# Kernel tuning notes

Hardware: AMD Instinct MI355X
Metric: run time of the kernel (lower is better)

## Reference

```python
import jax, jax.numpy as jnp
import numpy as np

LEAKY_SLOPE = 0.2  # tf.nn.leaky_relu default alpha
NEG_INF = -1e9


def setup_inputs() -> dict:
    key = jax.random.key(0)
    k1, k2, k3, k4 = jax.random.split(key, 4)
    B, N, F, D, H = 1, 4096, 128, 64, 4
    features = jax.random.normal(k1, (B, N, F), dtype=jnp.float32)
    adj = jax.random.randint(k2, (N, N), 0, 2, dtype=jnp.int32)  # 0/1 adjacency
    W = jax.random.normal(k3, (H, F, D), dtype=jnp.float32) * 0.1
    attn_k = jax.random.normal(k4, (H, 2 * D, 1), dtype=jnp.float32) * 0.1
    return {"adj": adj, "features": features, "W": W, "attn_k": attn_k}


def reference(adj, features, W, attn_k):
    H, _, D = W.shape
    adj_f = adj.astype(jnp.float32)[None]       # [1, N, N], broadcast over batch
    mask = adj_f != 0.0
    outs = []
    for i in range(H):  # fixed small head loop (heads are structurally distinct weights)
        h = features @ W[i]                      # [B, N, D]
        a_self = h @ attn_k[i, :D]               # [B, N, 1]
        a_neigh = h @ attn_k[i, D:]              # [B, N, 1]
        scores = a_self + jnp.swapaxes(a_neigh, 1, 2)  # [B, N, N] additive scores
        scores = jax.nn.leaky_relu(scores, LEAKY_SLOPE)
        scores = jnp.where(mask, scores, NEG_INF)
        attn = jax.nn.softmax(scores, axis=-1)   # [B, N, N]
        outs.append((attn * adj_f) @ h)          # [B, N, D]
    out = jnp.concatenate(outs, axis=-1) if H > 1 else outs[0]
    return jax.nn.relu(out)
```

## Files before the change

kernel.cpp:

```cpp
#include <hip/hip_runtime.h>
#include <math.h>

#define NN 4096
#define FF 128
#define DD 64
#define HH 4
#define NC 256

typedef _Float16 f16x8 __attribute__((ext_vector_type(8)));
typedef _Float16 f16x4 __attribute__((ext_vector_type(4)));
typedef _Float16 f16x2 __attribute__((ext_vector_type(2)));
typedef float    f32x4 __attribute__((ext_vector_type(4)));

__global__ __launch_bounds__(256) void prep_kernel(
    const float* __restrict__ feats, const float* __restrict__ W,
    const float* __restrict__ ak, _Float16* __restrict__ Bpack,
    _Float16* __restrict__ Es, _Float16* __restrict__ Fs,
    _Float16* __restrict__ En, _Float16* __restrict__ Fn)
{
    __shared__ _Float16 Wth[64 * 136];
    __shared__ _Float16 fth[32 * 128];
    __shared__ float    hlds[32 * 65];
    const int t  = threadIdx.x;
    const int h  = blockIdx.y;
    const int n0 = blockIdx.x * 32;

    {
        const float* Wh = W + h * (FF * DD);
        #pragma unroll
        for (int j = 0; j < 8; ++j) {
            int idx = j * 256 + t;
            int f   = idx >> 4;
            int d4  = idx & 15;
            float4 v = ((const float4*)Wh)[idx];
            Wth[(d4 * 4 + 0) * 136 + f] = (_Float16)v.x;
            Wth[(d4 * 4 + 1) * 136 + f] = (_Float16)v.y;
            Wth[(d4 * 4 + 2) * 136 + f] = (_Float16)v.z;
            Wth[(d4 * 4 + 3) * 136 + f] = (_Float16)v.w;
        }
        #pragma unroll
        for (int j = 0; j < 4; ++j) {
            int idx = j * 256 + t;
            int r = idx >> 5, f4 = idx & 31;
            float4 v = ((const float4*)feats)[(size_t)(n0 + r) * 32 + f4];
            f16x4 hv = {(_Float16)v.x, (_Float16)v.y, (_Float16)v.z, (_Float16)v.w};
            *(f16x4*)&fth[r * 128 + f4 * 4] = hv;
        }
    }
    __syncthreads();

    const int d   = t & 63;
    const int wid = t >> 6;
    float acc[8];
    #pragma unroll
    for (int j = 0; j < 8; ++j) acc[j] = 0.f;

    union UW { f16x8 v; unsigned int u[4]; };
    for (int f8 = 0; f8 < 16; ++f8) {
        UW w8; w8.v = *(const f16x8*)&Wth[d * 136 + f8 * 8];
        #pragma unroll
        for (int j = 0; j < 8; ++j) {
            const int r = wid + 4 * j;
            UW fv; fv.v = *(const f16x8*)&fth[r * 128 + f8 * 8];
            #pragma unroll
            for (int p = 0; p < 4; ++p)
                acc[j] = __builtin_amdgcn_fdot2(
                    __builtin_bit_cast(f16x2, w8.u[p]),
                    __builtin_bit_cast(f16x2, fv.u[p]), acc[j], false);
        }
    }

    const float aks = ak[h * 128 + d];
    const float akn = ak[h * 128 + 64 + d];
    #pragma unroll
    for (int j = 0; j < 8; ++j) {
        const int r = wid + 4 * j;
        const float hv = acc[j];
        hlds[r * 65 + d] = hv;
        float v1 = hv * aks;
        float v2 = hv * akn;
        #pragma unroll
        for (int m = 32; m >= 1; m >>= 1) {
            v1 += __shfl_xor(v1, m, 64);
            v2 += __shfl_xor(v2, m, 64);
        }
        if (d == 0) {
            Es[h * NN + n0 + r] = (_Float16)__expf(v1);
            Fs[h * NN + n0 + r] = (_Float16)__expf(0.2f * v1);
            En[h * NN + n0 + r] = (_Float16)__expf(v2);
            Fn[h * NN + n0 + r] = (_Float16)__expf(0.2f * v2);
        }
    }
    __syncthreads();

    const int cb = t >> 6;
    const int l  = t & 63;
    const int lr = l & 15;
    const int kg = l >> 4;
    f16x8 v;
    #pragma unroll
    for (int j = 0; j < 8; ++j)
        v[j] = (_Float16)hlds[(kg * 8 + j) * 65 + cb * 16 + lr];
    *(f16x8*)(Bpack + ((size_t)(h * 128 + blockIdx.x)) * 2048 + (cb * 64 + l) * 8) = v;
}

__global__ __launch_bounds__(256, 4) void attn_kernel(
    const int* __restrict__ adj, const _Float16* __restrict__ Bpack,
    const _Float16* __restrict__ Es, const _Float16* __restrict__ Fs,
    const _Float16* __restrict__ En, const _Float16* __restrict__ Fn,
    float* __restrict__ pacc, float* __restrict__ pden, int ksplit)
{
    __shared__ _Float16 adjh[2][2][1024];

    const int t  = threadIdx.x;
    const int h  = t >> 6;
    const int l  = t & 63;
    const int lr = l & 15;
    const int kg = l >> 4;
    const int n0 = blockIdx.x * 32;
    const int s  = blockIdx.y;

    const int mstart = s * ksplit;
    const int nch    = ksplit >> 5;
    const int coff   = blockIdx.x & (nch - 1);
#define PCH(c) ((((c) + coff) & (nch - 1)))
#define CLC(c) ((c) < nch ? (c) : nch - 1)

    const _Float16 es0 = Es[h * NN + n0 + lr],      fs0 = Fs[h * NN + n0 + lr];
    const _Float16 es1 = Es[h * NN + n0 + 16 + lr], fs1 = Fs[h * NN + n0 + 16 + lr];
    const f16x2 es20 = {es0, es0}, fs20 = {fs0, fs0};
    const f16x2 es21 = {es1, es1}, fs21 = {fs1, fs1};

    const _Float16* __restrict__ EnB = En + (size_t)h * NN + mstart + kg * 8;
    const _Float16* __restrict__ FnB = Fn + (size_t)h * NN + mstart + kg * 8;
    const _Float16* __restrict__ bhead =
        Bpack + ((size_t)(h * 128) + (mstart >> 5)) * 2048 + l * 8;

    const int sr = t >> 3;
    const int mq = t & 7;
    const int swoff = sr * 32 + (((mq >> 1) ^ (sr & 3)) << 3) + (mq & 1) * 4;
    const int* __restrict__ adjRow = adj + (size_t)(n0 + sr) * NN + mstart;

    const int perm = kg ^ (lr & 3);
    const int ro0  = lr * 32 + perm * 8;
    const int ro1  = (lr + 16) * 32 + perm * 8;

    f32x4 acc[2][4] = {};
    f32x4 dacc[2]   = {};
    f16x8 ones;
    #pragma unroll
    for (int j = 0; j < 8; ++j) ones[j] = (_Float16)1.0f;

    union U8 { f16x8 v; unsigned int u[4]; };

#define LDADJ(DST, C) do {                                                    \
        DST = ((const int4*)(adjRow + PCH(CLC(C)) * 32))[mq];                 \
    } while (0)
#define STADJ(PB, SUB, SRC) do {                                              \
        f16x4 _hv = {(_Float16)(SRC.x != 0), (_Float16)(SRC.y != 0),          \
                     (_Float16)(SRC.z != 0), (_Float16)(SRC.w != 0)};         \
        *(f16x4*)&adjh[PB][SUB][swoff] = _hv;                                 \
    } while (0)
#define LOADB(DST, C) do {                                                    \
        const _Float16* _b = bhead + (size_t)PCH(CLC(C)) * 2048;              \
        _Pragma("unroll")                                                     \
        for (int _cb = 0; _cb < 4; ++_cb)                                     \
            DST[_cb] = *(const f16x8*)(_b + _cb * 512);                       \
    } while (0)
#define LOADT(EQ, FQ, C) do {                                                 \
        EQ = *(const uint4*)(EnB + PCH(CLC(C)) * 32);                         \
        FQ = *(const uint4*)(FnB + PCH(CLC(C)) * 32);                         \
    } while (0)

#define CHUNK(C, PB, SUB, BCUR, BNXT, EQC, FQC, EQN, FQN) do {                \
        LOADB(BNXT, (C) + 1);                                                 \
        LOADT(EQN, FQN, (C) + 1);                                             \
        U8 AM0, AM1;                                                          \
        AM0.v = *(const f16x8*)&adjh[PB][SUB][ro0];                           \
        AM1.v = *(const f16x8*)&adjh[PB][SUB][ro1];                           \
        U8 A0, A1;                                                            \
        _Pragma("unroll")                                                     \
        for (int p = 0; p < 4; ++p) {                                         \
            const unsigned int eu = p == 0 ? EQC.x : p == 1 ? EQC.y : p == 2 ? EQC.z : EQC.w; \
            const unsigned int fu = p == 0 ? FQC.x : p == 1 ? FQC.y : p == 2 ? FQC.z : FQC.w; \
            const f16x2 en2 = __builtin_bit_cast(f16x2, eu);                  \
            const f16x2 fn2 = __builtin_bit_cast(f16x2, fu);                  \
            const f16x2 a20 = __builtin_bit_cast(f16x2, AM0.u[p]);            \
            const f16x2 a21 = __builtin_bit_cast(f16x2, AM1.u[p]);            \
            const f16x2 v0 = __builtin_elementwise_max(es20 * en2, fs20 * fn2) * a20; \
            const f16x2 v1 = __builtin_elementwise_max(es21 * en2, fs21 * fn2) * a21; \
            A0.u[p] = __builtin_bit_cast(unsigned int, v0);                   \
            A1.u[p] = __builtin_bit_cast(unsigned int, v1);                   \
        }                                                                     \
        __builtin_amdgcn_s_setprio(1);                                        \
        _Pragma("unroll")                                                     \
        for (int _cb = 0; _cb < 4; ++_cb) {                                   \
            acc[0][_cb] = __builtin_amdgcn_mfma_f32_16x16x32_f16(A0.v, BCUR[_cb], acc[0][_cb], 0, 0, 0); \
            acc[1][_cb] = __builtin_amdgcn_mfma_f32_16x16x32_f16(A1.v, BCUR[_cb], acc[1][_cb], 0, 0, 0); \
        }                                                                     \
        dacc[0] = __builtin_amdgcn_mfma_f32_16x16x32_f16(A0.v, ones, dacc[0], 0, 0, 0); \
        dacc[1] = __builtin_amdgcn_mfma_f32_16x16x32_f16(A1.v, ones, dacc[1], 0, 0, 0); \
        __builtin_amdgcn_s_setprio(0);                                        \
    } while (0)

    f16x8 B_0[4], B_1[4];
    uint4 eq0, fq0, eq1, fq1;
    int4  aA, aB;

    LDADJ(aA, 0);
    LDADJ(aB, 1);
    STADJ(0, 0, aA);
    STADJ(0, 1, aB);
    LDADJ(aA, 2);
    LDADJ(aB, 3);
    LOADB(B_0, 0);
    LOADT(eq0, fq0, 0);
    __syncthreads();

    const int npair = nch >> 1;
    for (int k = 0; k < npair; ++k) {
        const int nb = (k + 1) & 1;
        const int pb = k & 1;
        STADJ(nb, 0, aA);
        STADJ(nb, 1, aB);
        LDADJ(aA, 2 * k + 4);
        LDADJ(aB, 2 * k + 5);

        CHUNK(2 * k,     pb, 0, B_0, B_1, eq0, fq0, eq1, fq1);
        CHUNK(2 * k + 1, pb, 1, B_1, B_0, eq1, fq1, eq0, fq0);

        __syncthreads();
    }
#undef CHUNK
#undef LOADT
#undef LOADB
#undef STADJ
#undef LDADJ
#undef CLC
#undef PCH

    #pragma unroll
    for (int rb = 0; rb < 2; ++rb) {
        #pragma unroll
        for (int r = 0; r < 4; ++r) {
            const int row = n0 + rb * 16 + kg * 4 + r;
            #pragma unroll
            for (int cb = 0; cb < 4; ++cb)
                pacc[((size_t)(s * NN + row)) * NC + h * 64 + cb * 16 + lr] = acc[rb][cb][r];
            if (lr == 0)
                pden[(s * NN + row) * 4 + h] = dacc[rb][r];
        }
    }
}

__global__ __launch_bounds__(256) void finalize_kernel(
    const float* __restrict__ pacc, const float* __restrict__ pden,
    float* __restrict__ out, int nsplit)
{
    const int t = threadIdx.x;
    const int n = blockIdx.x * 4 + (t >> 6);
    const int q = t & 63;
    const int h = q >> 4;

    f32x4 a = {0.f, 0.f, 0.f, 0.f};
    float d = 0.f;
    for (int s = 0; s < nsplit; ++s) {
        a += *(const f32x4*)&pacc[((size_t)(s * NN + n)) * NC + q * 4];
        d += pden[(s * NN + n) * 4 + h];
    }
    f32x4 o;
    const float inv = (d > 0.f) ? 1.0f / d : 0.f;
    #pragma unroll
    for (int i = 0; i < 4; ++i) {
        const float v = a[i] * inv;
        o[i] = v > 0.f ? v : 0.f;
    }
    *(f32x4*)&out[(size_t)n * NC + q * 4] = o;
}

extern "C" void kernel_launch(void* const* d_in, const int* in_sizes, int n_in,
                              void* d_out, int out_size, void* d_ws, size_t ws_size,
                              hipStream_t stream)
{
    const int*   adj   = (const int*)d_in[0];
    const float* feats = (const float*)d_in[1];
    const float* W     = (const float*)d_in[2];
    const float* ak    = (const float*)d_in[3];
    float*       out   = (float*)d_out;

    char* ws = (char*)d_ws;
    _Float16* Bpack = (_Float16*)ws;
    _Float16* Es    = (_Float16*)(ws + (2ull << 20));
    _Float16* Fs    = (_Float16*)(ws + (2ull << 20) + (1 << 15));
    _Float16* En    = (_Float16*)(ws + (2ull << 20) + (2 << 15));
    _Float16* Fn    = (_Float16*)(ws + (2ull << 20) + (3 << 15));
    float*    pden  = (float*)(ws + (2ull << 20) + (4 << 15));
    float*    pacc  = (float*)(ws + (3ull << 20));

    int nsplit = 8;
    while (nsplit > 1 && ws_size < (3ull << 20) + (size_t)nsplit * (4ull << 20))
        nsplit >>= 1;
    const int ksplit = NN / nsplit;

    prep_kernel<<<dim3(128, 4), 256, 0, stream>>>(feats, W, ak, Bpack, Es, Fs, En, Fn);
    attn_kernel<<<dim3(128, nsplit), 256, 0, stream>>>(adj, Bpack, Es, Fs, En, Fn,
                                                       pacc, pden, ksplit);
    finalize_kernel<<<1024, 256, 0, stream>>>(pacc, pden, out, nsplit);
}
```

Measured before the change: 57.14 us.

## Store split partials in fp16, deepen adjacency prefetch, and load B per chunk

Partial accumulators and denominators are now written as fp16 instead of fp32, which halves the split-K partial traffic and the workspace footprint. The exp factors are pre-scaled by 1/8 so the fp16 partials stay in range, and finalize reads 8 halves per thread over fewer blocks. The attention loop now keeps four adjacency register stages in flight instead of two, while B and exp-factor loads are issued inside each chunk with no register double-buffering. The changes risk fp16 precision loss in the partial sums and expose B-load latency to the MFMA chain, though they cut register pressure.

```diff
diff --git a/kernel.cpp b/kernel.cpp
--- a/kernel.cpp
+++ b/kernel.cpp
@@ -6,6 +6,7 @@
 #define DD 64
 #define HH 4
 #define NC 256
+#define TSCALE 0.125f
 
 typedef _Float16 f16x8 __attribute__((ext_vector_type(8)));
 typedef _Float16 f16x4 __attribute__((ext_vector_type(4)));
@@ -85,10 +86,10 @@
             v2 += __shfl_xor(v2, m, 64);
         }
         if (d == 0) {
-            Es[h * NN + n0 + r] = (_Float16)__expf(v1);
-            Fs[h * NN + n0 + r] = (_Float16)__expf(0.2f * v1);
-            En[h * NN + n0 + r] = (_Float16)__expf(v2);
-            Fn[h * NN + n0 + r] = (_Float16)__expf(0.2f * v2);
+            Es[h * NN + n0 + r] = (_Float16)(__expf(v1) * TSCALE);
+            Fs[h * NN + n0 + r] = (_Float16)(__expf(0.2f * v1) * TSCALE);
+            En[h * NN + n0 + r] = (_Float16)(__expf(v2) * TSCALE);
+            Fn[h * NN + n0 + r] = (_Float16)(__expf(0.2f * v2) * TSCALE);
         }
     }
     __syncthreads();
@@ -108,7 +109,7 @@
     const int* __restrict__ adj, const _Float16* __restrict__ Bpack,
     const _Float16* __restrict__ Es, const _Float16* __restrict__ Fs,
     const _Float16* __restrict__ En, const _Float16* __restrict__ Fn,
-    float* __restrict__ pacc, float* __restrict__ pden, int ksplit)
+    _Float16* __restrict__ pacc, _Float16* __restrict__ pden, int ksplit)
 {
     __shared__ _Float16 adjh[2][2][1024];
 
@@ -161,28 +162,23 @@
                      (_Float16)(SRC.z != 0), (_Float16)(SRC.w != 0)};         \
         *(f16x4*)&adjh[PB][SUB][swoff] = _hv;                                 \
     } while (0)
-#define LOADB(DST, C) do {                                                    \
+
+#define CHUNK(C, PB, SUB) do {                                                \
         const _Float16* _b = bhead + (size_t)PCH(CLC(C)) * 2048;              \
-        _Pragma("unroll")                                                     \
-        for (int _cb = 0; _cb < 4; ++_cb)                                     \
-            DST[_cb] = *(const f16x8*)(_b + _cb * 512);                       \
-    } while (0)
-#define LOADT(EQ, FQ, C) do {                                                 \
-        EQ = *(const uint4*)(EnB + PCH(CLC(C)) * 32);                         \
-        FQ = *(const uint4*)(FnB + PCH(CLC(C)) * 32);                         \
-    } while (0)
-
-#define CHUNK(C, PB, SUB, BCUR, BNXT, EQC, FQC, EQN, FQN) do {                \
-        LOADB(BNXT, (C) + 1);                                                 \
-        LOADT(EQN, FQN, (C) + 1);                                             \
+        f16x8 Bf0 = *(const f16x8*)(_b);                                      \
+        f16x8 Bf1 = *(const f16x8*)(_b + 512);                                \
+        f16x8 Bf2 = *(const f16x8*)(_b + 1024);                               \
+        f16x8 Bf3 = *(const f16x8*)(_b + 1536);                               \
+        const uint4 eq = *(const uint4*)(EnB + PCH(CLC(C)) * 32);             \
+        const uint4 fq = *(const uint4*)(FnB + PCH(CLC(C)) * 32);             \
         U8 AM0, AM1;                                                          \
         AM0.v = *(const f16x8*)&adjh[PB][SUB][ro0];                           \
         AM1.v = *(const f16x8*)&adjh[PB][SUB][ro1];                           \
         U8 A0, A1;                                                            \
         _Pragma("unroll")                                                     \
         for (int p = 0; p < 4; ++p) {                                         \
-            const unsigned int eu = p == 0 ? EQC.x : p == 1 ? EQC.y : p == 2 ? EQC.z : EQC.w; \
-            const unsigned int fu = p == 0 ? FQC.x : p == 1 ? FQC.y : p == 2 ? FQC.z : FQC.w; \
+            const unsigned int eu = p == 0 ? eq.x : p == 1 ? eq.y : p == 2 ? eq.z : eq.w; \
+            const unsigned int fu = p == 0 ? fq.x : p == 1 ? fq.y : p == 2 ? fq.z : fq.w; \
             const f16x2 en2 = __builtin_bit_cast(f16x2, eu);                  \
             const f16x2 fn2 = __builtin_bit_cast(f16x2, fu);                  \
             const f16x2 a20 = __builtin_bit_cast(f16x2, AM0.u[p]);            \
@@ -193,47 +189,52 @@
             A1.u[p] = __builtin_bit_cast(unsigned int, v1);                   \
         }                                                                     \
         __builtin_amdgcn_s_setprio(1);                                        \
-        _Pragma("unroll")                                                     \
-        for (int _cb = 0; _cb < 4; ++_cb) {                                   \
-            acc[0][_cb] = __builtin_amdgcn_mfma_f32_16x16x32_f16(A0.v, BCUR[_cb], acc[0][_cb], 0, 0, 0); \
-            acc[1][_cb] = __builtin_amdgcn_mfma_f32_16x16x32_f16(A1.v, BCUR[_cb], acc[1][_cb], 0, 0, 0); \
-        }                                                                     \
+        acc[0][0] = __builtin_amdgcn_mfma_f32_16x16x32_f16(A0.v, Bf0, acc[0][0], 0, 0, 0); \
+        acc[1][0] = __builtin_amdgcn_mfma_f32_16x16x32_f16(A1.v, Bf0, acc[1][0], 0, 0, 0); \
+        acc[0][1] = __builtin_amdgcn_mfma_f32_16x16x32_f16(A0.v, Bf1, acc[0][1], 0, 0, 0); \
+        acc[1][1] = __builtin_amdgcn_mfma_f32_16x16x32_f16(A1.v, Bf1, acc[1][1], 0, 0, 0); \
+        acc[0][2] = __builtin_amdgcn_mfma_f32_16x16x32_f16(A0.v, Bf2, acc[0][2], 0, 0, 0); \
+        acc[1][2] = __builtin_amdgcn_mfma_f32_16x16x32_f16(A1.v, Bf2, acc[1][2], 0, 0, 0); \
+        acc[0][3] = __builtin_amdgcn_mfma_f32_16x16x32_f16(A0.v, Bf3, acc[0][3], 0, 0, 0); \
+        acc[1][3] = __builtin_amdgcn_mfma_f32_16x16x32_f16(A1.v, Bf3, acc[1][3], 0, 0, 0); \
         dacc[0] = __builtin_amdgcn_mfma_f32_16x16x32_f16(A0.v, ones, dacc[0], 0, 0, 0); \
         dacc[1] = __builtin_amdgcn_mfma_f32_16x16x32_f16(A1.v, ones, dacc[1], 0, 0, 0); \
         __builtin_amdgcn_s_setprio(0);                                        \
     } while (0)
 
-    f16x8 B_0[4], B_1[4];
-    uint4 eq0, fq0, eq1, fq1;
-    int4  aA, aB;
-
-    LDADJ(aA, 0);
-    LDADJ(aB, 1);
-    STADJ(0, 0, aA);
-    STADJ(0, 1, aB);
-    LDADJ(aA, 2);
-    LDADJ(aB, 3);
-    LOADB(B_0, 0);
-    LOADT(eq0, fq0, 0);
+    int4 a0A, a0B, a1A, a1B, a2A, a2B, a3A, a3B;
+
+    LDADJ(a0A, 0); LDADJ(a0B, 1);
+    LDADJ(a1A, 2); LDADJ(a1B, 3);
+    LDADJ(a2A, 4); LDADJ(a2B, 5);
+    LDADJ(a3A, 6); LDADJ(a3B, 7);
+    STADJ(0, 0, a0A); STADJ(0, 1, a0B);
     __syncthreads();
 
     const int npair = nch >> 1;
-    for (int k = 0; k < npair; ++k) {
-        const int nb = (k + 1) & 1;
-        const int pb = k & 1;
-        STADJ(nb, 0, aA);
-        STADJ(nb, 1, aB);
-        LDADJ(aA, 2 * k + 4);
-        LDADJ(aB, 2 * k + 5);
-
-        CHUNK(2 * k,     pb, 0, B_0, B_1, eq0, fq0, eq1, fq1);
-        CHUNK(2 * k + 1, pb, 1, B_1, B_0, eq1, fq1, eq0, fq0);
-
+    for (int k = 0; k < npair; k += 4) {
+        STADJ(1, 0, a1A); STADJ(1, 1, a1B);
+        LDADJ(a0A, 2 * k + 8); LDADJ(a0B, 2 * k + 9);
+        CHUNK(2 * k,     0, 0);
+        CHUNK(2 * k + 1, 0, 1);
         __syncthreads();
+        STADJ(0, 0, a2A); STADJ(0, 1, a2B);
+        LDADJ(a1A, 2 * k + 10); LDADJ(a1B, 2 * k + 11);
+        CHUNK(2 * k + 2, 1, 0);
+        CHUNK(2 * k + 3, 1, 1);
+        __syncthreads();
+        STADJ(1, 0, a3A); STADJ(1, 1, a3B);
+        LDADJ(a2A, 2 * k + 12); LDADJ(a2B, 2 * k + 13);
+        CHUNK(2 * k + 4, 0, 0);
+        CHUNK(2 * k + 5, 0, 1);
+        __syncthreads();
+        STADJ(0, 0, a0A); STADJ(0, 1, a0B);
+        LDADJ(a3A, 2 * k + 14); LDADJ(a3B, 2 * k + 15);
+        CHUNK(2 * k + 6, 1, 0);
+        CHUNK(2 * k + 7, 1, 1);
+        __syncthreads();
     }
 #undef CHUNK
-#undef LOADT
-#undef LOADB
 #undef STADJ
 #undef LDADJ
 #undef CLC
@@ -246,36 +247,45 @@
             const int row = n0 + rb * 16 + kg * 4 + r;
             #pragma unroll
             for (int cb = 0; cb < 4; ++cb)
-                pacc[((size_t)(s * NN + row)) * NC + h * 64 + cb * 16 + lr] = acc[rb][cb][r];
+                pacc[((size_t)(s * NN + row)) * NC + h * 64 + cb * 16 + lr] =
+                    (_Float16)acc[rb][cb][r];
             if (lr == 0)
-                pden[(s * NN + row) * 4 + h] = dacc[rb][r];
+                pden[(s * NN + row) * 4 + h] = (_Float16)dacc[rb][r];
         }
     }
 }
 
 __global__ __launch_bounds__(256) void finalize_kernel(
-    const float* __restrict__ pacc, const float* __restrict__ pden,
+    const _Float16* __restrict__ pacc, const _Float16* __restrict__ pden,
     float* __restrict__ out, int nsplit)
 {
     const int t = threadIdx.x;
-    const int n = blockIdx.x * 4 + (t >> 6);
-    const int q = t & 63;
-    const int h = q >> 4;
-
-    f32x4 a = {0.f, 0.f, 0.f, 0.f};
+    const int n = blockIdx.x * 8 + (t >> 5);
+    const int q = t & 31;
+    const int h = q >> 3;
+
+    float a[8];
+    #pragma unroll
+    for (int i = 0; i < 8; ++i) a[i] = 0.f;
     float d = 0.f;
     for (int s = 0; s < nsplit; ++s) {
-        a += *(const f32x4*)&pacc[((size_t)(s * NN + n)) * NC + q * 4];
-        d += pden[(s * NN + n) * 4 + h];
-    }
-    f32x4 o;
+        const f16x8 v = *(const f16x8*)&pacc[((size_t)(s * NN + n)) * NC + q * 8];
+        #pragma unroll
+        for (int i = 0; i < 8; ++i) a[i] += (float)v[i];
+        d += (float)pden[(s * NN + n) * 4 + h];
+    }
     const float inv = (d > 0.f) ? 1.0f / d : 0.f;
+    f32x4 o0, o1;
     #pragma unroll
     for (int i = 0; i < 4; ++i) {
-        const float v = a[i] * inv;
-        o[i] = v > 0.f ? v : 0.f;
-    }
-    *(f32x4*)&out[(size_t)n * NC + q * 4] = o;
+        const float v0 = a[i] * inv;
+        const float v1 = a[i + 4] * inv;
+        o0[i] = v0 > 0.f ? v0 : 0.f;
+        o1[i] = v1 > 0.f ? v1 : 0.f;
+    }
+    float* po = &out[(size_t)n * NC + q * 8];
+    *(f32x4*)po       = o0;
+    *(f32x4*)(po + 4) = o1;
 }
 
 extern "C" void kernel_launch(void* const* d_in, const int* in_sizes, int n_in,
@@ -294,16 +304,16 @@
     _Float16* Fs    = (_Float16*)(ws + (2ull << 20) + (1 << 15));
     _Float16* En    = (_Float16*)(ws + (2ull << 20) + (2 << 15));
     _Float16* Fn    = (_Float16*)(ws + (2ull << 20) + (3 << 15));
-    float*    pden  = (float*)(ws + (2ull << 20) + (4 << 15));
-    float*    pacc  = (float*)(ws + (3ull << 20));
+    _Float16* pden  = (_Float16*)(ws + (2ull << 20) + (4 << 15));
+    _Float16* pacc  = (_Float16*)(ws + (3ull << 20));
 
     int nsplit = 8;
-    while (nsplit > 1 && ws_size < (3ull << 20) + (size_t)nsplit * (4ull << 20))
+    while (nsplit > 1 && ws_size < (3ull << 20) + (size_t)nsplit * (2ull << 20))
         nsplit >>= 1;
     const int ksplit = NN / nsplit;
 
     prep_kernel<<<dim3(128, 4), 256, 0, stream>>>(feats, W, ak, Bpack, Es, Fs, En, Fn);
     attn_kernel<<<dim3(128, nsplit), 256, 0, stream>>>(adj, Bpack, Es, Fs, En, Fn,
                                                        pacc, pden, ksplit);
-    finalize_kernel<<<1024, 256, 0, stream>>>(pacc, pden, out, nsplit);
+    finalize_kernel<<<512, 256, 0, stream>>>(pacc, pden, out, nsplit);
 }
```

Result: slower. 67.26 us (+17.7%).

## Store split-K partials in fp16 and raise split count to sixteen

Applied to the files above, without the earlier changes.

The attention kernel's partial accumulators and denominators are now written as fp16 instead of fp32, with the exp factors prescaled by 0.125 to keep the partial sums inside fp16 range. Halving the partial buffer size lets the split-K count grow from 8 to 16 within the same workspace, which gives more blocks for parallelism. The finalize kernel reads f16x8 vectors and handles 8 columns per thread. The cost is reduced precision in the partial sums, a risk of fp16 overflow, and twice as many partials to reduce in finalize.

```diff
diff --git a/kernel.cpp b/kernel.cpp
--- a/kernel.cpp
+++ b/kernel.cpp
@@ -6,6 +6,7 @@
 #define DD 64
 #define HH 4
 #define NC 256
+#define TSCALE 0.125f
 
 typedef _Float16 f16x8 __attribute__((ext_vector_type(8)));
 typedef _Float16 f16x4 __attribute__((ext_vector_type(4)));
@@ -85,10 +86,10 @@
             v2 += __shfl_xor(v2, m, 64);
         }
         if (d == 0) {
-            Es[h * NN + n0 + r] = (_Float16)__expf(v1);
-            Fs[h * NN + n0 + r] = (_Float16)__expf(0.2f * v1);
-            En[h * NN + n0 + r] = (_Float16)__expf(v2);
-            Fn[h * NN + n0 + r] = (_Float16)__expf(0.2f * v2);
+            Es[h * NN + n0 + r] = (_Float16)(__expf(v1) * TSCALE);
+            Fs[h * NN + n0 + r] = (_Float16)(__expf(0.2f * v1) * TSCALE);
+            En[h * NN + n0 + r] = (_Float16)(__expf(v2) * TSCALE);
+            Fn[h * NN + n0 + r] = (_Float16)(__expf(0.2f * v2) * TSCALE);
         }
     }
     __syncthreads();
@@ -108,7 +109,7 @@
     const int* __restrict__ adj, const _Float16* __restrict__ Bpack,
     const _Float16* __restrict__ Es, const _Float16* __restrict__ Fs,
     const _Float16* __restrict__ En, const _Float16* __restrict__ Fn,
-    float* __restrict__ pacc, float* __restrict__ pden, int ksplit)
+    _Float16* __restrict__ pacc, _Float16* __restrict__ pden, int ksplit)
 {
     __shared__ _Float16 adjh[2][2][1024];
 
@@ -246,36 +247,45 @@
             const int row = n0 + rb * 16 + kg * 4 + r;
             #pragma unroll
             for (int cb = 0; cb < 4; ++cb)
-                pacc[((size_t)(s * NN + row)) * NC + h * 64 + cb * 16 + lr] = acc[rb][cb][r];
+                pacc[((size_t)(s * NN + row)) * NC + h * 64 + cb * 16 + lr] =
+                    (_Float16)acc[rb][cb][r];
             if (lr == 0)
-                pden[(s * NN + row) * 4 + h] = dacc[rb][r];
+                pden[(s * NN + row) * 4 + h] = (_Float16)dacc[rb][r];
         }
     }
 }
 
 __global__ __launch_bounds__(256) void finalize_kernel(
-    const float* __restrict__ pacc, const float* __restrict__ pden,
+    const _Float16* __restrict__ pacc, const _Float16* __restrict__ pden,
     float* __restrict__ out, int nsplit)
 {
     const int t = threadIdx.x;
-    const int n = blockIdx.x * 4 + (t >> 6);
-    const int q = t & 63;
-    const int h = q >> 4;
-
-    f32x4 a = {0.f, 0.f, 0.f, 0.f};
+    const int n = blockIdx.x * 8 + (t >> 5);
+    const int q = t & 31;
+    const int h = q >> 3;
+
+    float a[8];
+    #pragma unroll
+    for (int i = 0; i < 8; ++i) a[i] = 0.f;
     float d = 0.f;
     for (int s = 0; s < nsplit; ++s) {
-        a += *(const f32x4*)&pacc[((size_t)(s * NN + n)) * NC + q * 4];
-        d += pden[(s * NN + n) * 4 + h];
-    }
-    f32x4 o;
+        const f16x8 v = *(const f16x8*)&pacc[((size_t)(s * NN + n)) * NC + q * 8];
+        #pragma unroll
+        for (int i = 0; i < 8; ++i) a[i] += (float)v[i];
+        d += (float)pden[(s * NN + n) * 4 + h];
+    }
     const float inv = (d > 0.f) ? 1.0f / d : 0.f;
+    f32x4 o0, o1;
     #pragma unroll
     for (int i = 0; i < 4; ++i) {
-        const float v = a[i] * inv;
-        o[i] = v > 0.f ? v : 0.f;
-    }
-    *(f32x4*)&out[(size_t)n * NC + q * 4] = o;
+        const float v0 = a[i] * inv;
+        const float v1 = a[i + 4] * inv;
+        o0[i] = v0 > 0.f ? v0 : 0.f;
+        o1[i] = v1 > 0.f ? v1 : 0.f;
+    }
+    float* po = &out[(size_t)n * NC + q * 8];
+    *(f32x4*)po       = o0;
+    *(f32x4*)(po + 4) = o1;
 }
 
 extern "C" void kernel_launch(void* const* d_in, const int* in_sizes, int n_in,
@@ -294,16 +304,16 @@
     _Float16* Fs    = (_Float16*)(ws + (2ull << 20) + (1 << 15));
     _Float16* En    = (_Float16*)(ws + (2ull << 20) + (2 << 15));
     _Float16* Fn    = (_Float16*)(ws + (2ull << 20) + (3 << 15));
-    float*    pden  = (float*)(ws + (2ull << 20) + (4 << 15));
-    float*    pacc  = (float*)(ws + (3ull << 20));
-
-    int nsplit = 8;
-    while (nsplit > 1 && ws_size < (3ull << 20) + (size_t)nsplit * (4ull << 20))
+    _Float16* pden  = (_Float16*)(ws + (2ull << 20) + (4 << 15));
+    _Float16* pacc  = (_Float16*)(ws + (3ull << 20));
+
+    int nsplit = 16;
+    while (nsplit > 1 && ws_size < (3ull << 20) + (size_t)nsplit * (2ull << 20))
         nsplit >>= 1;
     const int ksplit = NN / nsplit;
 
     prep_kernel<<<dim3(128, 4), 256, 0, stream>>>(feats, W, ak, Bpack, Es, Fs, En, Fn);
     attn_kernel<<<dim3(128, nsplit), 256, 0, stream>>>(adj, Bpack, Es, Fs, En, Fn,
                                                        pacc, pden, ksplit);
-    finalize_kernel<<<1024, 256, 0, stream>>>(pacc, pden, out, nsplit);
+    finalize_kernel<<<512, 256, 0, stream>>>(pacc, pden, out, nsplit);
 }
```

Measured after the change: 64.39 us. 1.13x slower.
